# Kernel tuning notes

Hardware: AMD Instinct MI355X
Metric: run time of the kernel (lower is better)

## Reference

```python
import jax, jax.numpy as jnp
import numpy as np

H = 16      # num_heads
D = 64      # head_dim
BQ = 64     # block_size_q
BKV = 64    # block_size_kv


def setup_inputs() -> dict:
    key = jax.random.key(0)
    ks = jax.random.split(key, 5)
    B, S, dim = 2, 2048, 1024
    x = jax.random.normal(ks[0], (B, S, dim), dtype=jnp.float32)
    Wq = jax.random.normal(ks[1], (dim, H * D), dtype=jnp.float32) * 0.02
    Wk = jax.random.normal(ks[2], (dim, H * D), dtype=jnp.float32) * 0.02
    Wv = jax.random.normal(ks[3], (dim, H * D), dtype=jnp.float32) * 0.02
    Wo = jax.random.normal(ks[4], (H * D, dim), dtype=jnp.float32) * 0.02
    return {"x": x, "Wq": Wq, "Wk": Wk, "Wv": Wv, "Wo": Wo}


def _flash_tiled(q, k, v, scale):
    # q,k,v: (B, H, S, D). Non-causal tiled attention with online softmax,
    # faithfully replicating the source's per-iteration division by l_new.
    B, nh, S, d = q.shape
    nq, nkv = S // BQ, S // BKV
    qb = q.reshape(B, nh, nq, BQ, d)                       # all q blocks at once (outer loop vectorized)
    kb = k.reshape(B, nh, nkv, BKV, d).transpose(2, 0, 1, 3, 4)  # (nkv, B, H, BKV, D)
    vb = v.reshape(B, nh, nkv, BKV, d).transpose(2, 0, 1, 3, 4)

    o0 = jnp.zeros((B, nh, nq, BQ, d), q.dtype)
    m0 = jnp.full((B, nh, nq, BQ), -jnp.inf, q.dtype)
    l0 = jnp.zeros((B, nh, nq, BQ), q.dtype)

    def step(carry, kv):
        o, m, l = carry
        kj, vj = kv
        s = jnp.einsum('bhnqd,bhkd->bhnqk', qb, kj) * scale   # (B,H,nq,BQ,BKV)
        m_new = jnp.maximum(m, s.max(axis=-1))
        p = jnp.exp(s - m_new[..., None])
        alpha = jnp.exp(m - m_new)
        l_new = alpha * l + p.sum(axis=-1)
        # NOTE: division by l_new every iteration, as in the source module.
        o_new = (alpha[..., None] * o + jnp.einsum('bhnqk,bhkd->bhnqd', p, vj)) / l_new[..., None]
        return (o_new, m_new, l_new), None

    (o, _, _), _ = jax.lax.scan(step, (o0, m0, l0), (kb, vb))
    return o.reshape(B, nh, S, d)


def reference(x, Wq, Wk, Wv, Wo):
    B, S, dim = x.shape
    scale = D ** -0.5
    q = (x @ Wq).reshape(B, S, H, D).transpose(0, 2, 1, 3)
    k = (x @ Wk).reshape(B, S, H, D).transpose(0, 2, 1, 3)
    v = (x @ Wv).reshape(B, S, H, D).transpose(0, 2, 1, 3)
    o = _flash_tiled(q, k, v, scale)                       # (B,H,S,D)
    out = o.transpose(0, 2, 1, 3).reshape(B, S, H * D)
    return out @ Wo
```

## Files before the change

### kernel.cpp

```cpp
#include <hip/hip_runtime.h>
#include <hip/hip_bf16.h>
#include <math.h>

#define BB   2
#define SS   2048
#define DIM  1024
#define NH   16
#define HD   64
#define MTOT (BB * SS)

typedef unsigned short ushortT;
typedef __attribute__((ext_vector_type(8))) short short8v;
typedef __attribute__((ext_vector_type(4))) float float4v;

union FragU { short8v v; unsigned short us[8]; unsigned int u[4]; };

__device__ inline unsigned short f2bf(float x) {
    unsigned u = __builtin_bit_cast(unsigned, x);
    u += 0x7fffu + ((u >> 16) & 1u);
    return (unsigned short)(u >> 16);
}
__device__ inline float bf2f(unsigned short h) {
    unsigned u = ((unsigned)h) << 16;
    return __builtin_bit_cast(float, u);
}
__device__ inline void split_tr(float x, unsigned short& hi, unsigned short& lo) {
    unsigned u = __builtin_bit_cast(unsigned, x);
    hi = (unsigned short)(u >> 16);
    float hf = __builtin_bit_cast(float, u & 0xffff0000u);
    lo = (unsigned short)(__builtin_bit_cast(unsigned, x - hf) >> 16);
}
__device__ inline void split4(const float4& x, short4& hi, short4& lo) {
    unsigned short h0 = f2bf(x.x), h1 = f2bf(x.y), h2 = f2bf(x.z), h3 = f2bf(x.w);
    hi = make_short4((short)h0, (short)h1, (short)h2, (short)h3);
    lo = make_short4((short)f2bf(x.x - bf2f(h0)), (short)f2bf(x.y - bf2f(h1)),
                     (short)f2bf(x.z - bf2f(h2)), (short)f2bf(x.w - bf2f(h3)));
}
__device__ inline void gld_lds16(const void* g, void* l) {
    __builtin_amdgcn_global_load_lds(
        (const __attribute__((address_space(1))) void*)g,
        (__attribute__((address_space(3))) void*)l, 16, 0, 0);
}

__global__ __launch_bounds__(256) void convert_split_kernel(
    const float* __restrict__ in, ushortT* __restrict__ hi, ushortT* __restrict__ lo, int n4)
{
    int t = blockIdx.x * 256 + threadIdx.x;
    if (t < n4) {
        float4 x = ((const float4*)in)[t];
        short4 h, l; split4(x, h, l);
        ((short4*)hi)[t] = h;
        ((short4*)lo)[t] = l;
    }
}

__global__ __launch_bounds__(256) void transpose_split_kernel(
    const float* __restrict__ W0, const float* __restrict__ W1,
    const float* __restrict__ W2, const float* __restrict__ W3,
    ushortT* __restrict__ WtH, ushortT* __restrict__ WtL)
{
    const int z = blockIdx.z;
    const float* __restrict__ W = (z == 0) ? W0 : (z == 1) ? W1 : (z == 2) ? W2 : W3;
    ushortT* H = WtH + (size_t)z * 1024 * 1024;
    ushortT* L = WtL + (size_t)z * 1024 * 1024;

    __shared__ float T[64][65];
    const int k0 = blockIdx.y * 64, n0 = blockIdx.x * 64;
    const int tid = threadIdx.x;
    const int c4 = (tid & 15) * 4;

#pragma unroll
    for (int i = 0; i < 4; i++) {
        int r = (tid >> 4) + 16 * i;
        *(float4*)&T[r][c4] = *(const float4*)(W + (size_t)(k0 + r) * 1024 + n0 + c4);
    }
    __syncthreads();
#pragma unroll
    for (int i = 0; i < 4; i++) {
        int n = (tid >> 4) + 16 * i;
        float4 vv = make_float4(T[c4 + 0][n], T[c4 + 1][n], T[c4 + 2][n], T[c4 + 3][n]);
        short4 h, l; split4(vv, h, l);
        *(short4*)&H[(size_t)(n0 + n) * 1024 + k0 + c4] = h;
        *(short4*)&L[(size_t)(n0 + n) * 1024 + k0 + c4] = l;
    }
}

__global__ __launch_bounds__(256) void kv_convert_kernel(
    const float* __restrict__ kw,
    ushortT* __restrict__ KhG, ushortT* __restrict__ KlG)
{
    const int jb = blockIdx.x, bh = blockIdx.y;
    const int b = bh >> 4, h = bh & 15;

    __shared__ float T[64][68];
    const int tid = threadIdx.x;
    const size_t ibase = (size_t)b * SS * DIM + (size_t)h * HD + (size_t)(jb * 64) * DIM;
    const int c4 = (tid & 15) * 4;
#pragma unroll
    for (int i = 0; i < 4; i++) {
        int r = (tid >> 4) + 16 * i;
        *(float4*)&T[r][c4] = *(const float4*)(kw + ibase + (size_t)r * DIM + c4);
    }
    __syncthreads();

    ushortT* oh = KhG + (size_t)(bh * 32 + jb) * 4096;
    ushortT* ol = KlG + (size_t)(bh * 32 + jb) * 4096;

#pragma unroll
    for (int i = 0; i < 2; i++) {
        const int s = tid + i * 256;
        const int f = s >> 6;
        const int lane = s & 63;
        const int ks = f >> 2, c = f & 3;
        const int qd = lane >> 4, l15 = lane & 15;
        const int kv = c * 16 + l15;
        const int d0 = ks * 32 + qd * 8;
        ushortT hv[8], lv[8];
#pragma unroll
        for (int j = 0; j < 8; j++) split_tr(T[kv][d0 + j], hv[j], lv[j]);
        *(short4*)&oh[s * 8]     = *(short4*)&hv[0];
        *(short4*)&oh[s * 8 + 4] = *(short4*)&hv[4];
        *(short4*)&ol[s * 8]     = *(short4*)&lv[0];
        *(short4*)&ol[s * 8 + 4] = *(short4*)&lv[4];
    }
}

__global__ __launch_bounds__(256, 2) void gemm_bt_split_kernel(
    const ushortT* __restrict__ Ah, const ushortT* __restrict__ Al,
    const ushortT* __restrict__ BtH, const ushortT* __restrict__ BtL,
    float* __restrict__ Y0, float* __restrict__ Y1,
    ushortT* __restrict__ VhG, ushortT* __restrict__ VlG)
{
    const int z = blockIdx.z;
    const ushortT* __restrict__ Bh = BtH + (size_t)z * 1024 * 1024;
    const ushortT* __restrict__ Bl = BtL + (size_t)z * 1024 * 1024;

    const int K = 1024, N = 1024;
    const int m0 = blockIdx.y * 128;
    const int n0 = blockIdx.x * 128;

    __shared__ __align__(16) ushortT AhS[128 * 32];
    __shared__ __align__(16) ushortT AlS[128 * 32];
    __shared__ __align__(16) ushortT BhS[128 * 32];
    __shared__ __align__(16) ushortT BlS[128 * 32];

    const int tid  = threadIdx.x;
    const int wave = tid >> 6, lane = tid & 63;
    const int quad = lane >> 4, l15 = lane & 15;
    const int wm = wave >> 1, wn = wave & 1;

    const int s0 = tid, s1 = tid + 256;
    const int ar0 = s0 >> 2, ak0 = (s0 & 3) * 8;
    const int ar1 = s1 >> 2, ak1 = (s1 & 3) * 8;

    float4v acc[4][4];
#pragma unroll
    for (int i = 0; i < 4; i++)
#pragma unroll
        for (int j = 0; j < 4; j++) acc[i][j] = (float4v){0.f, 0.f, 0.f, 0.f};

    for (int k0 = 0; k0 < K; k0 += 32) {
        __syncthreads();
        gld_lds16(Ah + (size_t)(m0 + ar0) * K + k0 + ak0, &AhS[s0 * 8]);
        gld_lds16(Ah + (size_t)(m0 + ar1) * K + k0 + ak1, &AhS[s1 * 8]);
        gld_lds16(Al + (size_t)(m0 + ar0) * K + k0 + ak0, &AlS[s0 * 8]);
        gld_lds16(Al + (size_t)(m0 + ar1) * K + k0 + ak1, &AlS[s1 * 8]);
        gld_lds16(Bh + (size_t)(n0 + ar0) * K + k0 + ak0, &BhS[s0 * 8]);
        gld_lds16(Bh + (size_t)(n0 + ar1) * K + k0 + ak1, &BhS[s1 * 8]);
        gld_lds16(Bl + (size_t)(n0 + ar0) * K + k0 + ak0, &BlS[s0 * 8]);
        gld_lds16(Bl + (size_t)(n0 + ar1) * K + k0 + ak1, &BlS[s1 * 8]);
        __syncthreads();

        FragU ah[4], al[4], bh[4], bl[4];
#pragma unroll
        for (int t = 0; t < 4; t++) {
            ah[t].v = *(const short8v*)&AhS[(wm * 64 + t * 16 + l15) * 32 + quad * 8];
            al[t].v = *(const short8v*)&AlS[(wm * 64 + t * 16 + l15) * 32 + quad * 8];
            bh[t].v = *(const short8v*)&BhS[(wn * 64 + t * 16 + l15) * 32 + quad * 8];
            bl[t].v = *(const short8v*)&BlS[(wn * 64 + t * 16 + l15) * 32 + quad * 8];
        }
#pragma unroll
        for (int mt = 0; mt < 4; mt++)
#pragma unroll
            for (int nt = 0; nt < 4; nt++) {
                acc[mt][nt] = __builtin_amdgcn_mfma_f32_16x16x32_bf16(ah[mt].v, bh[nt].v, acc[mt][nt], 0, 0, 0);
                acc[mt][nt] = __builtin_amdgcn_mfma_f32_16x16x32_bf16(ah[mt].v, bl[nt].v, acc[mt][nt], 0, 0, 0);
                acc[mt][nt] = __builtin_amdgcn_mfma_f32_16x16x32_bf16(al[mt].v, bh[nt].v, acc[mt][nt], 0, 0, 0);
            }
    }

    if (z == 2) {
        const int b  = m0 >> 11;
        const int jb = ((m0 & 2047) >> 6) + wm;
        const int h  = (n0 >> 6) + wn;
        const size_t tb = (size_t)((b * 16 + h) * 32 + jb) * 4096;
        ushortT* vh = VhG + tb;
        ushortT* vl = VlG + tb;
#pragma unroll
        for (int mt = 0; mt < 4; mt++)
#pragma unroll
            for (int nt = 0; nt < 4; nt++) {
                const int off = ((((mt >> 1) * 4 + nt) * 64 +
                                  ((mt & 1) * 2 + (quad >> 1)) * 16 + l15) * 8) +
                                (quad & 1) * 4;
                float4 vv = make_float4(acc[mt][nt][0], acc[mt][nt][1],
                                        acc[mt][nt][2], acc[mt][nt][3]);
                unsigned short h0, l0, h1, l1, h2, l2, h3, l3;
                split_tr(vv.x, h0, l0); split_tr(vv.y, h1, l1);
                split_tr(vv.z, h2, l2); split_tr(vv.w, h3, l3);
                *(short4*)&vh[off] = make_short4((short)h0, (short)h1, (short)h2, (short)h3);
                *(short4*)&vl[off] = make_short4((short)l0, (short)l1, (short)l2, (short)l3);
            }
    } else {
        float* __restrict__ Y = (z == 0) ? Y0 : Y1;
#pragma unroll
        for (int mt = 0; mt < 4; mt++)
#pragma unroll
            for (int r = 0; r < 4; r++) {
                const int row = m0 + wm * 64 + mt * 16 + quad * 4 + r;
                float* yp = Y + (size_t)row * N + n0 + wn * 64 + l15;
#pragma unroll
                for (int nt = 0; nt < 4; nt++)
                    yp[nt * 16] = acc[mt][nt][r];
            }
    }
}

__global__ __launch_bounds__(256, 2) void attn_mfma_kernel(
    const float* __restrict__ q,
    const ushortT* __restrict__ KhG, const ushortT* __restrict__ KlG,
    const ushortT* __restrict__ VhG, const ushortT* __restrict__ VlG,
    ushortT* __restrict__ Oh, ushortT* __restrict__ Ol)
{
    __shared__ __align__(16) ushortT KhS[4096];
    __shared__ __align__(16) ushortT KlS[4096];
    __shared__ __align__(16) ushortT VhS[4096];
    __shared__ __align__(16) ushortT VlS[4096];
    __shared__ __align__(16) ushortT PW[4][2][2048];

    const int tid  = threadIdx.x;
    const int wave = tid >> 6, lane = tid & 63;
    const int quad = lane >> 4, l15 = lane & 15;
    const int bh = blockIdx.y, b = bh >> 4, h = bh & 15;
    const size_t base = (size_t)b * SS * DIM + (size_t)h * HD;
    const int qs0 = blockIdx.x * 128 + wave * 32;

    const float qscale = 0.125f * 1.4426950408889634f;
    FragU Qh[2][2], Ql[2][2];
#pragma unroll
    for (int rt = 0; rt < 2; rt++) {
        const int qrow = qs0 + rt * 16 + l15;
#pragma unroll
        for (int ks = 0; ks < 2; ks++) {
            const float* p0 = q + base + (size_t)qrow * DIM + ks * 32 + quad * 8;
            float4 a = *(const float4*)(p0);
            float4 c = *(const float4*)(p0 + 4);
            float e[8] = {a.x, a.y, a.z, a.w, c.x, c.y, c.z, c.w};
#pragma unroll
            for (int j = 0; j < 8; j++) {
                float x = e[j] * qscale;
                unsigned short hs = f2bf(x);
                Qh[rt][ks].us[j] = hs;
                Ql[rt][ks].us[j] = f2bf(x - bf2f(hs));
            }
        }
    }

    float4v Oacc[4][2];
#pragma unroll
    for (int dt = 0; dt < 4; dt++)
#pragma unroll
        for (int rt = 0; rt < 2; rt++) Oacc[dt][rt] = (float4v){0.f, 0.f, 0.f, 0.f};

    float m_run[2] = {-INFINITY, -INFINITY};
    float l_run[2] = {0.f, 0.f};

    const int sl0 = wave * 128 + lane, sl1 = sl0 + 64;
    ushortT* ph = &PW[wave][0][0];
    ushortT* pl = &PW[wave][1][0];
    const int pwq = ((quad >> 1) * 16 + l15) * 8 + (quad & 1) * 4;
    const int lane8 = lane * 8;

    for (int jb = 0; jb < 32; jb++) {
        __syncthreads();
        {
            const size_t tb = (size_t)(bh * 32 + jb) * 4096;
            gld_lds16(KhG + tb + sl0 * 8, &KhS[sl0 * 8]);
            gld_lds16(KhG + tb + sl1 * 8, &KhS[sl1 * 8]);
            gld_lds16(KlG + tb + sl0 * 8, &KlS[sl0 * 8]);
            gld_lds16(KlG + tb + sl1 * 8, &KlS[sl1 * 8]);
            gld_lds16(VhG + tb + sl0 * 8, &VhS[sl0 * 8]);
            gld_lds16(VhG + tb + sl1 * 8, &VhS[sl1 * 8]);
            gld_lds16(VlG + tb + sl0 * 8, &VlS[sl0 * 8]);
            gld_lds16(VlG + tb + sl1 * 8, &VlS[sl1 * 8]);
        }
        __syncthreads();

        float4v st[4][2];
#pragma unroll
        for (int mt = 0; mt < 4; mt++)
#pragma unroll
            for (int rt = 0; rt < 2; rt++) st[mt][rt] = (float4v){0.f, 0.f, 0.f, 0.f};

#pragma unroll
        for (int ks = 0; ks < 2; ks++) {
            FragU kh[4], kl[4];
#pragma unroll
            for (int mt = 0; mt < 4; mt++) {
                kh[mt].v = *(const short8v*)&KhS[((ks * 4 + mt) * 64) * 8 + lane8];
                kl[mt].v = *(const short8v*)&KlS[((ks * 4 + mt) * 64) * 8 + lane8];
            }
#pragma unroll
            for (int mt = 0; mt < 4; mt++)
#pragma unroll
                for (int rt = 0; rt < 2; rt++) {
                    st[mt][rt] = __builtin_amdgcn_mfma_f32_16x16x32_bf16(kh[mt].v, Qh[rt][ks].v, st[mt][rt], 0, 0, 0);
                    st[mt][rt] = __builtin_amdgcn_mfma_f32_16x16x32_bf16(kh[mt].v, Ql[rt][ks].v, st[mt][rt], 0, 0, 0);
                    st[mt][rt] = __builtin_amdgcn_mfma_f32_16x16x32_bf16(kl[mt].v, Qh[rt][ks].v, st[mt][rt], 0, 0, 0);
                }
        }

        float oscale[2];
#pragma unroll
        for (int rt = 0; rt < 2; rt++) {
            float v0 = fmaxf(fmaxf(st[0][rt][0], st[0][rt][1]), fmaxf(st[0][rt][2], st[0][rt][3]));
#pragma unroll
            for (int mt = 1; mt < 4; mt++) {
                float v1 = fmaxf(fmaxf(st[mt][rt][0], st[mt][rt][1]), fmaxf(st[mt][rt][2], st[mt][rt][3]));
                v0 = fmaxf(v0, v1);
            }
            v0 = fmaxf(v0, __shfl_xor(v0, 16, 64));
            v0 = fmaxf(v0, __shfl_xor(v0, 32, 64));
            const float mn = fmaxf(m_run[rt], v0);
            const float al = __builtin_amdgcn_exp2f(m_run[rt] - mn);

            float ssum = 0.f;
#pragma unroll
            for (int mt = 0; mt < 4; mt++)
#pragma unroll
                for (int r = 0; r < 4; r++) {
                    const float p = __builtin_amdgcn_exp2f(st[mt][rt][r] - mn);
                    st[mt][rt][r] = p;
                    ssum += p;
                }
            ssum += __shfl_xor(ssum, 16, 64);
            ssum += __shfl_xor(ssum, 32, 64);
            const float ln = al * l_run[rt] + ssum;
            const float inv = __builtin_amdgcn_rcpf(ln);
            oscale[rt] = al * inv;
#pragma unroll
            for (int mt = 0; mt < 4; mt++)
#pragma unroll
                for (int r = 0; r < 4; r++)
                    st[mt][rt][r] *= inv;
            m_run[rt] = mn;
            l_run[rt] = ln;
        }

#pragma unroll
        for (int rt = 0; rt < 2; rt++)
#pragma unroll
            for (int mt = 0; mt < 4; mt++) {
                unsigned u0 = __builtin_bit_cast(unsigned, st[mt][rt][0]);
                unsigned u1 = __builtin_bit_cast(unsigned, st[mt][rt][1]);
                unsigned u2 = __builtin_bit_cast(unsigned, st[mt][rt][2]);
                unsigned u3 = __builtin_bit_cast(unsigned, st[mt][rt][3]);
                unsigned h01 = (u0 >> 16) | (u1 & 0xffff0000u);
                unsigned h23 = (u2 >> 16) | (u3 & 0xffff0000u);
                float d0 = st[mt][rt][0] - __builtin_bit_cast(float, u0 & 0xffff0000u);
                float d1 = st[mt][rt][1] - __builtin_bit_cast(float, u1 & 0xffff0000u);
                float d2 = st[mt][rt][2] - __builtin_bit_cast(float, u2 & 0xffff0000u);
                float d3 = st[mt][rt][3] - __builtin_bit_cast(float, u3 & 0xffff0000u);
                unsigned l01 = (__builtin_bit_cast(unsigned, d0) >> 16) |
                               (__builtin_bit_cast(unsigned, d1) & 0xffff0000u);
                unsigned l23 = (__builtin_bit_cast(unsigned, d2) >> 16) |
                               (__builtin_bit_cast(unsigned, d3) & 0xffff0000u);
                const int idx = ((rt * 2 + (mt >> 1)) * 512 + (mt & 1) * 256) + pwq;
                *(uint2*)&ph[idx] = make_uint2(h01, h23);
                *(uint2*)&pl[idx] = make_uint2(l01, l23);
            }

        FragU Ph[2][2], Pl[2][2];
#pragma unroll
        for (int rt = 0; rt < 2; rt++)
#pragma unroll
            for (int ks = 0; ks < 2; ks++) {
                Ph[rt][ks].v = *(const short8v*)&ph[((rt * 2 + ks) * 64) * 8 + lane8];
                Pl[rt][ks].v = *(const short8v*)&pl[((rt * 2 + ks) * 64) * 8 + lane8];
            }

#pragma unroll
        for (int dt = 0; dt < 4; dt++)
#pragma unroll
            for (int rt = 0; rt < 2; rt++)
#pragma unroll
                for (int r = 0; r < 4; r++)
                    Oacc[dt][rt][r] *= oscale[rt];

#pragma unroll
        for (int ks = 0; ks < 2; ks++)
#pragma unroll
            for (int dt = 0; dt < 4; dt++) {
                FragU vh, vl;
                vh.v = *(const short8v*)&VhS[((ks * 4 + dt) * 64) * 8 + lane8];
                vl.v = *(const short8v*)&VlS[((ks * 4 + dt) * 64) * 8 + lane8];
#pragma unroll
                for (int rt = 0; rt < 2; rt++) {
                    Oacc[dt][rt] = __builtin_amdgcn_mfma_f32_16x16x32_bf16(vh.v, Ph[rt][ks].v, Oacc[dt][rt], 0, 0, 0);
                    Oacc[dt][rt] = __builtin_amdgcn_mfma_f32_16x16x32_bf16(vl.v, Ph[rt][ks].v, Oacc[dt][rt], 0, 0, 0);
                    Oacc[dt][rt] = __builtin_amdgcn_mfma_f32_16x16x32_bf16(vh.v, Pl[rt][ks].v, Oacc[dt][rt], 0, 0, 0);
                }
            }
    }

    float* Pf = (float*)&PW[wave][0][0];
    const int q16 = lane >> 2, c = lane & 3;
#pragma unroll
    for (int rt = 0; rt < 2; rt++) {
#pragma unroll
        for (int dt = 0; dt < 4; dt++)
            *(float4v*)&Pf[l15 * 68 + dt * 16 + quad * 4] = Oacc[dt][rt];
        float vals[16];
#pragma unroll
        for (int kk = 0; kk < 4; kk++)
            *(float4v*)&vals[kk * 4] = *(const float4v*)&Pf[q16 * 68 + c * 16 + kk * 4];

        unsigned ho[8], lo8[8];
#pragma unroll
        for (int kk = 0; kk < 8; kk++) {
            unsigned short h0, l0, h1, l1;
            split_tr(vals[2 * kk], h0, l0);
            split_tr(vals[2 * kk + 1], h1, l1);
            ho[kk]  = (unsigned)h0 | ((unsigned)h1 << 16);
            lo8[kk] = (unsigned)l0 | ((unsigned)l1 << 16);
        }
        const int qrow = qs0 + rt * 16 + q16;
        const size_t off = (size_t)(b * SS + qrow) * DIM + h * HD + c * 16;
        *(uint4*)&Oh[off]     = make_uint4(ho[0], ho[1], ho[2], ho[3]);
        *(uint4*)&Oh[off + 8] = make_uint4(ho[4], ho[5], ho[6], ho[7]);
        *(uint4*)&Ol[off]     = make_uint4(lo8[0], lo8[1], lo8[2], lo8[3]);
        *(uint4*)&Ol[off + 8] = make_uint4(lo8[4], lo8[5], lo8[6], lo8[7]);
    }
}

extern "C" void kernel_launch(void* const* d_in, const int* in_sizes, int n_in,
                              void* d_out, int out_size, void* d_ws, size_t ws_size,
                              hipStream_t stream)
{
    const float* x  = (const float*)d_in[0];
    const float* Wq = (const float*)d_in[1];
    const float* Wk = (const float*)d_in[2];
    const float* Wv = (const float*)d_in[3];
    const float* Wo = (const float*)d_in[4];
    float* out = (float*)d_out;

    char* w = (char*)d_ws;
    float*   qw  = (float*)(w);
    float*   kw  = (float*)(w + ((size_t)16 << 20));
    ushortT* VhG = (ushortT*)(w + ((size_t)32 << 20));
    ushortT* VlG = (ushortT*)(w + ((size_t)40 << 20));
    ushortT* XhS = (ushortT*)(w + ((size_t)48 << 20));
    ushortT* XlS = (ushortT*)(w + ((size_t)56 << 20));
    ushortT* WtH = (ushortT*)(w + ((size_t)64 << 20));
    ushortT* WtL = (ushortT*)(w + ((size_t)72 << 20));
    ushortT* KhG = (ushortT*)(w + ((size_t)80 << 20));
    ushortT* KlG = (ushortT*)(w + ((size_t)88 << 20));
    ushortT* OhS = (ushortT*)kw;
    ushortT* OlS = (ushortT*)(w + ((size_t)24 << 20));

    dim3 blk(256);
    const int n4 = MTOT * DIM / 4;

    convert_split_kernel<<<dim3(n4 / 256), blk, 0, stream>>>(x, XhS, XlS, n4);
    transpose_split_kernel<<<dim3(16, 16, 4), blk, 0, stream>>>(Wq, Wk, Wv, Wo, WtH, WtL);

    gemm_bt_split_kernel<<<dim3(8, 32, 3), blk, 0, stream>>>(
        XhS, XlS, WtH, WtL, qw, kw, VhG, VlG);

    kv_convert_kernel<<<dim3(32, 32), blk, 0, stream>>>(kw, KhG, KlG);

    attn_mfma_kernel<<<dim3(16, 32), blk, 0, stream>>>(qw, KhG, KlG, VhG, VlG, OhS, OlS);

    gemm_bt_split_kernel<<<dim3(8, 32, 1), blk, 0, stream>>>(
        OhS, OlS, WtH + (size_t)3 * 1024 * 1024, WtL + (size_t)3 * 1024 * 1024,
        out, nullptr, nullptr, nullptr);
}
```

Before: 332.3 us.

## Double-buffer K/V tiles in LDS and prefetch the next block during compute

The attention kernel now keeps two LDS buffers for the K/V hi/lo tiles. It issues the global-to-LDS loads for block jb+1 right after the barrier, then computes on block jb, which drops one of the two barriers per iteration and hides load latency behind the MFMA work. The per-wave P scratch is halved by reusing it across the two row tiles, and the epilogue's float staging moves into the now-idle first K/V buffer. Total LDS rises to about 80KB per block, which with two blocks per CU sits right at the LDS capacity and could limit occupancy.

```diff
diff --git a/kernel.cpp b/kernel.cpp
--- a/kernel.cpp
+++ b/kernel.cpp
@@ -203,11 +203,9 @@
                 const int off = ((((mt >> 1) * 4 + nt) * 64 +
                                   ((mt & 1) * 2 + (quad >> 1)) * 16 + l15) * 8) +
                                 (quad & 1) * 4;
-                float4 vv = make_float4(acc[mt][nt][0], acc[mt][nt][1],
-                                        acc[mt][nt][2], acc[mt][nt][3]);
                 unsigned short h0, l0, h1, l1, h2, l2, h3, l3;
-                split_tr(vv.x, h0, l0); split_tr(vv.y, h1, l1);
-                split_tr(vv.z, h2, l2); split_tr(vv.w, h3, l3);
+                split_tr(acc[mt][nt][0], h0, l0); split_tr(acc[mt][nt][1], h1, l1);
+                split_tr(acc[mt][nt][2], h2, l2); split_tr(acc[mt][nt][3], h3, l3);
                 *(short4*)&vh[off] = make_short4((short)h0, (short)h1, (short)h2, (short)h3);
                 *(short4*)&vl[off] = make_short4((short)l0, (short)l1, (short)l2, (short)l3);
             }
@@ -232,11 +230,8 @@
     const ushortT* __restrict__ VhG, const ushortT* __restrict__ VlG,
     ushortT* __restrict__ Oh, ushortT* __restrict__ Ol)
 {
-    __shared__ __align__(16) ushortT KhS[4096];
-    __shared__ __align__(16) ushortT KlS[4096];
-    __shared__ __align__(16) ushortT VhS[4096];
-    __shared__ __align__(16) ushortT VlS[4096];
-    __shared__ __align__(16) ushortT PW[4][2][2048];
+    __shared__ __align__(16) ushortT KVS[2][4][4096];
+    __shared__ __align__(16) ushortT PW[4][2048];
 
     const int tid  = threadIdx.x;
     const int wave = tid >> 6, lane = tid & 63;
@@ -276,25 +271,44 @@
     float l_run[2] = {0.f, 0.f};
 
     const int sl0 = wave * 128 + lane, sl1 = sl0 + 64;
-    ushortT* ph = &PW[wave][0][0];
-    ushortT* pl = &PW[wave][1][0];
+    const int lane8 = lane * 8;
+    ushortT* ph = &PW[wave][0];
+    ushortT* pl = &PW[wave][1024];
     const int pwq = ((quad >> 1) * 16 + l15) * 8 + (quad & 1) * 4;
-    const int lane8 = lane * 8;
+
+    {
+        const size_t tb = (size_t)(bh * 32) * 4096;
+        ushortT* B = &KVS[0][0][0];
+        gld_lds16(KhG + tb + sl0 * 8, B + sl0 * 8);
+        gld_lds16(KhG + tb + sl1 * 8, B + sl1 * 8);
+        gld_lds16(KlG + tb + sl0 * 8, B + 4096 + sl0 * 8);
+        gld_lds16(KlG + tb + sl1 * 8, B + 4096 + sl1 * 8);
+        gld_lds16(VhG + tb + sl0 * 8, B + 8192 + sl0 * 8);
+        gld_lds16(VhG + tb + sl1 * 8, B + 8192 + sl1 * 8);
+        gld_lds16(VlG + tb + sl0 * 8, B + 12288 + sl0 * 8);
+        gld_lds16(VlG + tb + sl1 * 8, B + 12288 + sl1 * 8);
+    }
 
     for (int jb = 0; jb < 32; jb++) {
+        const int cur = jb & 1;
+        const ushortT* KhS = &KVS[cur][0][0];
+        const ushortT* KlS = &KVS[cur][1][0];
+        const ushortT* VhS = &KVS[cur][2][0];
+        const ushortT* VlS = &KVS[cur][3][0];
+
         __syncthreads();
-        {
-            const size_t tb = (size_t)(bh * 32 + jb) * 4096;
-            gld_lds16(KhG + tb + sl0 * 8, &KhS[sl0 * 8]);
-            gld_lds16(KhG + tb + sl1 * 8, &KhS[sl1 * 8]);
-            gld_lds16(KlG + tb + sl0 * 8, &KlS[sl0 * 8]);
-            gld_lds16(KlG + tb + sl1 * 8, &KlS[sl1 * 8]);
-            gld_lds16(VhG + tb + sl0 * 8, &VhS[sl0 * 8]);
-            gld_lds16(VhG + tb + sl1 * 8, &VhS[sl1 * 8]);
-            gld_lds16(VlG + tb + sl0 * 8, &VlS[sl0 * 8]);
-            gld_lds16(VlG + tb + sl1 * 8, &VlS[sl1 * 8]);
-        }
-        __syncthreads();
+        if (jb < 31) {
+            const size_t tb = (size_t)(bh * 32 + jb + 1) * 4096;
+            ushortT* B = &KVS[cur ^ 1][0][0];
+            gld_lds16(KhG + tb + sl0 * 8, B + sl0 * 8);
+            gld_lds16(KhG + tb + sl1 * 8, B + sl1 * 8);
+            gld_lds16(KlG + tb + sl0 * 8, B + 4096 + sl0 * 8);
+            gld_lds16(KlG + tb + sl1 * 8, B + 4096 + sl1 * 8);
+            gld_lds16(VhG + tb + sl0 * 8, B + 8192 + sl0 * 8);
+            gld_lds16(VhG + tb + sl1 * 8, B + 8192 + sl1 * 8);
+            gld_lds16(VlG + tb + sl0 * 8, B + 12288 + sl0 * 8);
+            gld_lds16(VlG + tb + sl1 * 8, B + 12288 + sl1 * 8);
+        }
 
         float4v st[4][2];
 #pragma unroll
@@ -321,6 +335,7 @@
         }
 
         float oscale[2];
+        FragU Ph[2][2], Pl[2][2];
 #pragma unroll
         for (int rt = 0; rt < 2; rt++) {
             float v0 = fmaxf(fmaxf(st[0][rt][0], st[0][rt][1]), fmaxf(st[0][rt][2], st[0][rt][3]));
@@ -355,10 +370,7 @@
                     st[mt][rt][r] *= inv;
             m_run[rt] = mn;
             l_run[rt] = ln;
-        }
-
-#pragma unroll
-        for (int rt = 0; rt < 2; rt++)
+
 #pragma unroll
             for (int mt = 0; mt < 4; mt++) {
                 unsigned u0 = __builtin_bit_cast(unsigned, st[mt][rt][0]);
@@ -375,19 +387,16 @@
                                (__builtin_bit_cast(unsigned, d1) & 0xffff0000u);
                 unsigned l23 = (__builtin_bit_cast(unsigned, d2) >> 16) |
                                (__builtin_bit_cast(unsigned, d3) & 0xffff0000u);
-                const int idx = ((rt * 2 + (mt >> 1)) * 512 + (mt & 1) * 256) + pwq;
+                const int idx = (mt >> 1) * 512 + (mt & 1) * 256 + pwq;
                 *(uint2*)&ph[idx] = make_uint2(h01, h23);
                 *(uint2*)&pl[idx] = make_uint2(l01, l23);
             }
-
-        FragU Ph[2][2], Pl[2][2];
-#pragma unroll
-        for (int rt = 0; rt < 2; rt++)
 #pragma unroll
             for (int ks = 0; ks < 2; ks++) {
-                Ph[rt][ks].v = *(const short8v*)&ph[((rt * 2 + ks) * 64) * 8 + lane8];
-                Pl[rt][ks].v = *(const short8v*)&pl[((rt * 2 + ks) * 64) * 8 + lane8];
-            }
+                Ph[rt][ks].v = *(const short8v*)&ph[ks * 512 + lane8];
+                Pl[rt][ks].v = *(const short8v*)&pl[ks * 512 + lane8];
+            }
+        }
 
 #pragma unroll
         for (int dt = 0; dt < 4; dt++)
@@ -413,7 +422,7 @@
             }
     }
 
-    float* Pf = (float*)&PW[wave][0][0];
+    float* Pf = (float*)&KVS[0][0][0] + (size_t)wave * 1088;
     const int q16 = lane >> 2, c = lane & 3;
 #pragma unroll
     for (int rt = 0; rt < 2; rt++) {
```

Result: no change. 333.6 us (+0.4%).
